# Performance work log

Measured on AMD Instinct MI355X. Metric: run time of the kernel, lower is better.

The kernel has to match this reference:

```python
import jax, jax.numpy as jnp
from jax import lax
import numpy as np

RADIUS = 0.1
NSAMPLE = 32
STRIDE = 4
NUM_DIR = 32
BN_EPS = 1e-5


def _fps(p, m):
    # furthest point sampling: p (B,N,3) -> (B,m) int32 indices, start at index 0
    B, N, _ = p.shape

    def step(carry, _):
        dists, last = carry
        lp = jnp.take_along_axis(p, jnp.broadcast_to(last[:, None, None], (B, 1, 3)), axis=1)
        d = jnp.sum((p - lp) ** 2, axis=-1)
        dists = jnp.minimum(dists, d)
        nxt = jnp.argmax(dists, axis=-1).astype(jnp.int32)
        return (dists, nxt), nxt

    last0 = jnp.zeros((B,), jnp.int32)
    d0 = jnp.full((B, N), 1e10, p.dtype)
    _, rest = lax.scan(step, (d0, last0), None, length=m - 1)
    return jnp.concatenate([last0[None, :], rest], axis=0).T  # (B, m)


def _ball_query(q, p, k, radius):
    # q (B,M,3) centers, p (B,N,3) support -> (B,M,k) indices of first k points in ball,
    # padded with the first found index (PointNet++ convention)
    N = p.shape[1]
    d2 = jnp.sum((q[:, :, None, :] - p[:, None, :, :]) ** 2, axis=-1)  # (B,M,N)
    cand = jnp.where(d2 < radius * radius, jnp.arange(N, dtype=jnp.int32), N)
    cand = jnp.sort(cand, axis=-1)[:, :, :k]
    first = cand[:, :, :1]
    return jnp.where(cand == N, first, cand)


def _bn(x, g, b, m, v):
    # BatchNorm1d eval mode on (B,C,N)
    return (x - m[:, None]) * (g[:, None] / jnp.sqrt(v[:, None] + BN_EPS)) + b[:, None]


def _normalize(x, axis):
    return x / jnp.maximum(jnp.linalg.norm(x, axis=axis, keepdims=True), 1e-12)


def setup_inputs() -> dict:
    key = jax.random.key(0)
    ks = jax.random.split(key, 16)
    B, N, Cin, Cout = 4, 8192, 128, 256
    half = Cout // 2
    s = 0.02
    return {
        "p": jax.random.uniform(ks[0], (B, N, 3), jnp.float32),
        "f": jax.random.normal(ks[1], (B, Cin, N), jnp.float32),
        "conv1_w": jax.random.normal(ks[2], (Cout, Cin), jnp.float32) * s,
        "conv1_b": jax.random.normal(ks[3], (Cout,), jnp.float32) * s,
        "skip_w": jax.random.normal(ks[4], (Cout, Cin), jnp.float32) * s,
        "skip_b": jax.random.normal(ks[5], (Cout,), jnp.float32) * s,
        "bn1_g": jnp.ones((Cout,), jnp.float32),
        "bn1_b": jnp.zeros((Cout,), jnp.float32),
        "bn1_m": jax.random.normal(ks[6], (Cout,), jnp.float32) * 0.1,
        "bn1_v": jax.random.uniform(ks[7], (Cout,), jnp.float32) + 0.5,
        "dir_vectors": jax.random.normal(ks[8], (NUM_DIR, 3), jnp.float32),
        "de_w1": jax.random.normal(ks[9], (half, NUM_DIR), jnp.float32) * s,
        "de_g": jnp.ones((half,), jnp.float32),
        "de_bb": jnp.zeros((half,), jnp.float32),
        "de_m": jax.random.normal(ks[10], (half,), jnp.float32) * 0.1,
        "de_v": jax.random.uniform(ks[11], (half,), jnp.float32) + 0.5,
        "de_w2": jax.random.normal(ks[12], (Cout, half), jnp.float32) * s,
        "de_b2": jax.random.normal(ks[13], (Cout,), jnp.float32) * s,
    }


def reference(p, f, conv1_w, conv1_b, skip_w, skip_b, bn1_g, bn1_b, bn1_m, bn1_v,
              dir_vectors, de_w1, de_g, de_bb, de_m, de_v, de_w2, de_b2):
    B, N, _ = p.shape
    Cout = conv1_w.shape[0]
    M, K = N // STRIDE, NSAMPLE

    # FPS sampling + centroid gather
    idx = _fps(p, M)  # (B,M)
    new_p = jnp.take_along_axis(p, jnp.broadcast_to(idx[:, :, None], (B, M, 3)), axis=1)

    # residual branch: gather input feats at centroids, 1x1 conv (bn_after=False)
    fi = jnp.take_along_axis(f, jnp.broadcast_to(idx[:, None, :], (B, f.shape[1], M)), axis=2)
    identity = jnp.einsum('oc,bcm->bom', skip_w, fi) + skip_b[:, None]

    # convs1: 1x1 conv on all N points
    f1 = jnp.einsum('oc,bcn->bon', conv1_w, f) + conv1_b[:, None]  # (B,Cout,N)

    # ball-query grouping
    qidx = _ball_query(new_p, p, K, RADIUS)  # (B,M,K)
    idxf = qidx.reshape(B, M * K)
    gp = jnp.take_along_axis(p, jnp.broadcast_to(idxf[:, :, None], (B, M * K, 3)), axis=1).reshape(B, M, K, 3)
    dp = jnp.transpose(gp - new_p[:, :, None, :], (0, 3, 1, 2))  # (B,3,M,K)
    fj = jnp.take_along_axis(f1, jnp.broadcast_to(idxf[:, None, :], (B, Cout, M * K)), axis=2).reshape(B, Cout, M, K)

    # directional encoding
    dpn = _normalize(dp, axis=1)
    vec = _normalize(dir_vectors, axis=1)  # (NUM_DIR,3)
    theta = jnp.einsum('md,bdnk->bmnk', vec, dpn)  # (B,NUM_DIR,M,K)
    tmax = theta.max(axis=-1)  # (B,NUM_DIR,M)
    h = jnp.einsum('om,bmn->bon', de_w1, tmax)
    h = jax.nn.gelu(_bn(h, de_g, de_bb, de_m, de_v), approximate=False)
    pe = jnp.einsum('oc,bcn->bon', de_w2, h) + de_b2[:, None]

    # neighbor max-pool + BN + residuals
    f_out = _bn(fj.max(axis=-1), bn1_g, bn1_b, bn1_m, bn1_v) + pe + identity
    return new_p, f_out
```

## Files before the change

### kernel.cpp

```cpp
#include <hip/hip_runtime.h>

#define BATCH 4
#define NPTS 8192
#define MPTS 2048
#define CIN 128
#define CO 256
#define KS 32
#define ND 32
#define HALF 128

typedef unsigned int u32;
typedef unsigned long long u64;

#define DPPC_QUAD_XOR1 0xB1
#define DPPC_QUAD_XOR2 0x4E
#define DPPC_ROW_MIRROR 0x140
#define DPPC_ROW_HALF_MIRROR 0x141
#define DPPC_ROW_BCAST15 0x142
#define DPPC_ROW_BCAST31 0x143

template<int CTRL>
__device__ __forceinline__ float dpp_max(float v) {
    int o = __builtin_amdgcn_update_dpp(__float_as_int(-1e30f), __float_as_int(v),
                                        CTRL, 0xF, 0xF, false);
    return fmaxf(v, __int_as_float(o));
}
__device__ __forceinline__ float wave_max_f32(float v) {
    v = dpp_max<DPPC_QUAD_XOR1>(v);
    v = dpp_max<DPPC_QUAD_XOR2>(v);
    v = dpp_max<DPPC_ROW_HALF_MIRROR>(v);
    v = dpp_max<DPPC_ROW_MIRROR>(v);
    v = dpp_max<DPPC_ROW_BCAST15>(v);
    v = dpp_max<DPPC_ROW_BCAST31>(v);
    return __int_as_float(__builtin_amdgcn_readlane(__float_as_int(v), 63));
}

__global__
__attribute__((amdgpu_flat_work_group_size(512, 512), amdgpu_waves_per_eu(2, 2)))
void k_fps_f1(
    const float* __restrict__ p, const float* __restrict__ f,
    const float* __restrict__ conv1_w, const float* __restrict__ conv1_b,
    float* __restrict__ out_newp, int* __restrict__ idx,
    float* __restrict__ f1t) {
    if (blockIdx.x < 4) {
        __shared__ u64 wkey[2][8];
        int b = blockIdx.x, t = threadIdx.x;
        int lane = t & 63, wid = t >> 6;
        int j0 = t * 16;
        const float* pb = p + (size_t)b * NPTS * 3;
        const float* pt = pb + t * 48;
        float px[16], py[16], pz[16], dist[16];
#pragma unroll
        for (int c = 0; c < 4; ++c) {
            float4 q0 = *(const float4*)(pt + c * 12 + 0);
            float4 q1 = *(const float4*)(pt + c * 12 + 4);
            float4 q2 = *(const float4*)(pt + c * 12 + 8);
            px[c*4+0] = q0.x; py[c*4+0] = q0.y; pz[c*4+0] = q0.z;
            px[c*4+1] = q0.w; py[c*4+1] = q1.x; pz[c*4+1] = q1.y;
            px[c*4+2] = q1.z; py[c*4+2] = q1.w; pz[c*4+2] = q2.x;
            px[c*4+3] = q2.y; py[c*4+3] = q2.z; pz[c*4+3] = q2.w;
        }
#pragma unroll
        for (int i = 0; i < 16; ++i) {
            asm volatile("" : "+v"(px[i]), "+v"(py[i]), "+v"(pz[i]));
        }
#pragma unroll
        for (int i = 0; i < 16; ++i) dist[i] = 1e10f;
        float lx = pb[0], ly = pb[1], lz = pb[2];
        if (t == 0) {
            out_newp[(size_t)b * MPTS * 3 + 0] = lx;
            out_newp[(size_t)b * MPTS * 3 + 1] = ly;
            out_newp[(size_t)b * MPTS * 3 + 2] = lz;
            idx[b * MPTS] = 0;
        }
        for (int s = 1; s < MPTS; ++s) {
            int par = s & 1;
            float bv = -1e30f; int bi = 0;
#pragma unroll
            for (int i = 0; i < 16; ++i) {
                float dx = __fsub_rn(px[i], lx);
                float dy = __fsub_rn(py[i], ly);
                float dz = __fsub_rn(pz[i], lz);
                float d  = __fadd_rn(__fadd_rn(__fmul_rn(dx, dx), __fmul_rn(dy, dy)),
                                     __fmul_rn(dz, dz));
                float nd = fminf(dist[i], d);
                dist[i] = nd;
                bool gt = nd > bv;
                bi = gt ? i : bi;
                bv = fmaxf(bv, nd);
            }
            float gmw = wave_max_f32(bv);
            u64 mask = __ballot(bv == gmw);
            int first = __ffsll((long long)mask) - 1;
            if (lane == first) {
                wkey[par][wid] = ((u64)__float_as_uint(gmw) << 32)
                               | (u64)(u32)(NPTS - 1 - (j0 + bi));
            }
            __syncthreads();
            u64 bestk = wkey[par][0];
#pragma unroll
            for (int ww = 1; ww < 8; ++ww) {
                u64 kk = wkey[par][ww];
                if (kk > bestk) bestk = kk;
            }
            int w0 = (NPTS - 1 - (int)(bestk & 0xFFFFFFFFull)) & (NPTS - 1);
            int w0s = __builtin_amdgcn_readfirstlane(w0);
            lx = pb[w0s * 3 + 0]; ly = pb[w0s * 3 + 1]; lz = pb[w0s * 3 + 2];
            if (t == 0) {
                idx[b * MPTS + s] = w0s;
                out_newp[((size_t)b * MPTS + s) * 3 + 0] = lx;
                out_newp[((size_t)b * MPTS + s) * 3 + 1] = ly;
                out_newp[((size_t)b * MPTS + s) * 3 + 2] = lz;
            }
        }
    } else if (f1t != nullptr) {
        __shared__ __align__(16) float fT[CIN * 32];
        int blk = blockIdx.x - 4;
        int b = blk >> 8;
        int n0 = (blk & 255) << 5;
        int t = threadIdx.x;
        const float* fb = f + (size_t)b * CIN * NPTS;
        for (int e = t; e < CIN * 32; e += 512) {
            int k = e >> 5, j = e & 31;
            fT[e] = fb[(size_t)k * NPTS + n0 + j];
        }
        __syncthreads();
        int c = t & 255, jh = (t >> 8) << 4;
        float bias = conv1_b[c];
        float acc[16];
#pragma unroll
        for (int j = 0; j < 16; ++j) acc[j] = bias;
        const float4* wrow4 = (const float4*)(conv1_w + (size_t)c * CIN);
        const float4* fT4 = (const float4*)fT;
        for (int k4 = 0; k4 < 32; ++k4) {
            float4 wv = wrow4[k4];
#pragma unroll
            for (int sub = 0; sub < 4; ++sub) {
                float w = sub == 0 ? wv.x : sub == 1 ? wv.y : sub == 2 ? wv.z : wv.w;
                int k = k4 * 4 + sub;
                int base = (k * 32 + jh) >> 2;
                float4 a0 = fT4[base+0], a1 = fT4[base+1], a2 = fT4[base+2], a3 = fT4[base+3];
                acc[0]  = fmaf(w, a0.x, acc[0]);  acc[1]  = fmaf(w, a0.y, acc[1]);
                acc[2]  = fmaf(w, a0.z, acc[2]);  acc[3]  = fmaf(w, a0.w, acc[3]);
                acc[4]  = fmaf(w, a1.x, acc[4]);  acc[5]  = fmaf(w, a1.y, acc[5]);
                acc[6]  = fmaf(w, a1.z, acc[6]);  acc[7]  = fmaf(w, a1.w, acc[7]);
                acc[8]  = fmaf(w, a2.x, acc[8]);  acc[9]  = fmaf(w, a2.y, acc[9]);
                acc[10] = fmaf(w, a2.z, acc[10]); acc[11] = fmaf(w, a2.w, acc[11]);
                acc[12] = fmaf(w, a3.x, acc[12]); acc[13] = fmaf(w, a3.y, acc[13]);
                acc[14] = fmaf(w, a3.z, acc[14]); acc[15] = fmaf(w, a3.w, acc[15]);
            }
        }
        float* dst = f1t + ((size_t)b * NPTS + n0 + jh) * CO + c;
#pragma unroll
        for (int j = 0; j < 16; ++j) dst[(size_t)j * CO] = acc[j];
    }
}

__global__ __launch_bounds__(256) void k_f1(const float* __restrict__ f,
                                            const float* __restrict__ conv1_w,
                                            const float* __restrict__ conv1_b,
                                            float* __restrict__ f1t, int b0) {
    __shared__ __align__(16) float fT[CIN * 16];
    int blk = blockIdx.x;
    int bl = blk >> 9;
    int b = b0 + bl;
    int n0 = (blk & 511) << 4;
    int t = threadIdx.x;
    const float* fb = f + (size_t)b * CIN * NPTS;
    for (int e = t; e < CIN * 16; e += 256) {
        int k = e >> 4, j = e & 15;
        fT[e] = fb[(size_t)k * NPTS + n0 + j];
    }
    __syncthreads();
    int c = t;
    float bias = conv1_b[c];
    float acc[16];
#pragma unroll
    for (int j = 0; j < 16; ++j) acc[j] = bias;
    const float4* wrow4 = (const float4*)(conv1_w + (size_t)c * CIN);
    const float4* fT4 = (const float4*)fT;
    for (int k4 = 0; k4 < 32; ++k4) {
        float4 wv = wrow4[k4];
#pragma unroll
        for (int sub = 0; sub < 4; ++sub) {
            float w = sub == 0 ? wv.x : sub == 1 ? wv.y : sub == 2 ? wv.z : wv.w;
            int k = k4 * 4 + sub;
            float4 a0 = fT4[k*4+0], a1 = fT4[k*4+1], a2 = fT4[k*4+2], a3 = fT4[k*4+3];
            acc[0]  = fmaf(w, a0.x, acc[0]);  acc[1]  = fmaf(w, a0.y, acc[1]);
            acc[2]  = fmaf(w, a0.z, acc[2]);  acc[3]  = fmaf(w, a0.w, acc[3]);
            acc[4]  = fmaf(w, a1.x, acc[4]);  acc[5]  = fmaf(w, a1.y, acc[5]);
            acc[6]  = fmaf(w, a1.z, acc[6]);  acc[7]  = fmaf(w, a1.w, acc[7]);
            acc[8]  = fmaf(w, a2.x, acc[8]);  acc[9]  = fmaf(w, a2.y, acc[9]);
            acc[10] = fmaf(w, a2.z, acc[10]); acc[11] = fmaf(w, a2.w, acc[11]);
            acc[12] = fmaf(w, a3.x, acc[12]); acc[13] = fmaf(w, a3.y, acc[13]);
            acc[14] = fmaf(w, a3.z, acc[14]); acc[15] = fmaf(w, a3.w, acc[15]);
        }
    }
    float* dst = f1t + ((size_t)bl * NPTS + n0) * CO + c;
#pragma unroll
    for (int j = 0; j < 16; ++j) dst[(size_t)j * CO] = acc[j];
}

__global__ __launch_bounds__(256) void k_feat(
    const float* __restrict__ p, const float* __restrict__ f,
    const float* __restrict__ f1t,
    const float* __restrict__ skip_w,  const float* __restrict__ skip_b,
    const float* __restrict__ bn1_g, const float* __restrict__ bn1_b,
    const float* __restrict__ bn1_m, const float* __restrict__ bn1_v,
    const float* __restrict__ dirv,  const float* __restrict__ de_w1,
    const float* __restrict__ de_g,  const float* __restrict__ de_bb,
    const float* __restrict__ de_m,  const float* __restrict__ de_v,
    const float* __restrict__ de_w2, const float* __restrict__ de_b2,
    const int* __restrict__ idx,     float* __restrict__ out_f, int b0) {
    __shared__ float sdx[KS], sdy[KS], sdz[KS];
    __shared__ float ltm[ND], lfi[CIN], lh[HALF];
    __shared__ int swidx[4][KS];
    __shared__ int scnt[4];
    __shared__ int nb[KS], nbp[KS];

    int q = b0 * MPTS + blockIdx.x;
    int b = q >> 11;
    int bl = b - b0;
    int m = q & (MPTS - 1);
    int t = threadIdx.x, lane = t & 63, w = t >> 6;
    const float* pb = p + (size_t)b * NPTS * 3;
    int i0 = idx[q] & (NPTS - 1);
    float qx = pb[i0 * 3 + 0], qy = pb[i0 * 3 + 1], qz = pb[i0 * 3 + 2];
    const float R2 = 0.1f * 0.1f;

    int cnt = 0;
    int seg = w * 2048;
    for (int base = 0; base < 2048; base += 64) {
        int j = seg + base + lane;
        float dx = __fsub_rn(pb[j * 3 + 0], qx);
        float dy = __fsub_rn(pb[j * 3 + 1], qy);
        float dz = __fsub_rn(pb[j * 3 + 2], qz);
        float d2 = __fadd_rn(__fadd_rn(__fmul_rn(dx, dx), __fmul_rn(dy, dy)),
                             __fmul_rn(dz, dz));
        bool hit = d2 < R2;
        u64 mask = __ballot(hit);
        if (hit) {
            int pos = cnt + __popcll(mask & ((1ull << lane) - 1ull));
            if (pos < KS) swidx[w][pos] = j;
        }
        cnt += __popcll(mask);
        if (cnt >= KS) break;
    }
    if (lane == 0) scnt[w] = cnt < KS ? cnt : KS;
    __syncthreads();
    int c0s = scnt[0], c1s = scnt[1], c2s = scnt[2], c3s = scnt[3];
    int st1 = c0s, st2 = c0s + c1s, st3 = c0s + c1s + c2s;
    int total = c0s + c1s + c2s + c3s; if (total > KS) total = KS;
    if (total < 1) total = 1;
    if (t < 128) {
        int ww = t >> 5, l = t & 31;
        int stw = (ww == 0) ? 0 : (ww == 1) ? st1 : (ww == 2) ? st2 : st3;
        int cw  = (ww == 0) ? c0s : (ww == 1) ? c1s : (ww == 2) ? c2s : c3s;
        int gp = stw + l;
        if (l < cw && gp < KS) nb[gp] = swidx[ww][l];
    }
    __syncthreads();
    if (t < KS) {
        int jk = nb[t < total ? t : 0] & (NPTS - 1);
        nbp[t] = jk;
        float dx = pb[jk * 3 + 0] - qx;
        float dy = pb[jk * 3 + 1] - qy;
        float dz = pb[jk * 3 + 2] - qz;
        float nr = fmaxf(sqrtf(dx * dx + dy * dy + dz * dz), 1e-12f);
        sdx[t] = dx / nr; sdy[t] = dy / nr; sdz[t] = dz / nr;
    }
    if (t >= 128) {
        lfi[t - 128] = f[((size_t)b * CIN + (t - 128)) * NPTS + i0];
    }
    __syncthreads();
    if (t < ND) {
        float ax = dirv[t * 3], ay = dirv[t * 3 + 1], az = dirv[t * 3 + 2];
        float n = fmaxf(sqrtf(ax * ax + ay * ay + az * az), 1e-12f);
        float vx = ax / n, vy = ay / n, vz = az / n;
        float tm = -1e30f;
#pragma unroll
        for (int k = 0; k < KS; ++k)
            tm = fmaxf(tm, vx * sdx[k] + vy * sdy[k] + vz * sdz[k]);
        ltm[t] = tm;
    }
    __syncthreads();

    int c = t;
    const float* f1b = f1t + (size_t)bl * NPTS * CO + c;
    float mx = -1e30f;
#pragma unroll 8
    for (int k = 0; k < KS; ++k) {
        mx = fmaxf(mx, f1b[(size_t)nbp[k] * CO]);
    }
    float sc1 = bn1_g[c] / sqrtf(bn1_v[c] + 1e-5f);
    float o1 = (mx - bn1_m[c]) * sc1 + bn1_b[c];

    float idv = skip_b[c];
    {
        const float4* sr = (const float4*)(skip_w + (size_t)c * CIN);
#pragma unroll 8
        for (int r = 0; r < 32; ++r) {
            float4 v = sr[r];
            idv = fmaf(v.x, lfi[r*4+0], fmaf(v.y, lfi[r*4+1],
                  fmaf(v.z, lfi[r*4+2], fmaf(v.w, lfi[r*4+3], idv))));
        }
    }
    {
        int hc = c & (HALF - 1);
        const float4* d1 = (const float4*)(de_w1 + (size_t)hc * ND);
        float a = 0.0f;
#pragma unroll
        for (int r = 0; r < 8; ++r) {
            float4 v = d1[r];
            a = fmaf(v.x, ltm[r*4+0], fmaf(v.y, ltm[r*4+1],
                fmaf(v.z, ltm[r*4+2], fmaf(v.w, ltm[r*4+3], a))));
        }
        float dsc = de_g[hc] / sqrtf(de_v[hc] + 1e-5f);
        float xb = (a - de_m[hc]) * dsc + de_bb[hc];
        float hv = 0.5f * xb * (1.0f + erff(xb * 0.70710678118654752440f));
        if (c < HALF) lh[c] = hv;
    }
    __syncthreads();
    float pe = de_b2[c];
    {
        const float4* d2p = (const float4*)(de_w2 + (size_t)c * HALF);
#pragma unroll 8
        for (int r = 0; r < 32; ++r) {
            float4 v = d2p[r];
            pe = fmaf(v.x, lh[r*4+0], fmaf(v.y, lh[r*4+1],
                 fmaf(v.z, lh[r*4+2], fmaf(v.w, lh[r*4+3], pe))));
        }
    }
    out_f[((size_t)b * CO + c) * MPTS + m] = o1 + pe + idv;
}

__global__ __launch_bounds__(256) void k_featz_fused(
    const float* __restrict__ p, const float* __restrict__ f,
    const float* __restrict__ conv1_w, const float* __restrict__ conv1_b,
    const float* __restrict__ skip_w,  const float* __restrict__ skip_b,
    const float* __restrict__ bn1_g, const float* __restrict__ bn1_b,
    const float* __restrict__ bn1_m, const float* __restrict__ bn1_v,
    const float* __restrict__ dirv,  const float* __restrict__ de_w1,
    const float* __restrict__ de_g,  const float* __restrict__ de_bb,
    const float* __restrict__ de_m,  const float* __restrict__ de_v,
    const float* __restrict__ de_w2, const float* __restrict__ de_b2,
    const int* __restrict__ idx,     float* __restrict__ out_f) {
    __shared__ __align__(16) float fg[KS * CIN];
    __shared__ float sdx[KS], sdy[KS], sdz[KS];
    __shared__ float ltm[ND], lfi[CIN], lh[HALF];
    __shared__ int swidx[4][KS];
    __shared__ int scnt[4];
    __shared__ int nb[KS], nbp[KS];

    int q = blockIdx.x;
    int b = q >> 11;
    int m = q & (MPTS - 1);
    int t = threadIdx.x, lane = t & 63, w = t >> 6;
    const float* pb = p + (size_t)b * NPTS * 3;
    int i0 = idx[q] & (NPTS - 1);
    float qx = pb[i0 * 3 + 0], qy = pb[i0 * 3 + 1], qz = pb[i0 * 3 + 2];
    const float R2 = 0.1f * 0.1f;
    int cnt = 0;
    int seg = w * 2048;
    for (int base = 0; base < 2048; base += 64) {
        int j = seg + base + lane;
        float dx = __fsub_rn(pb[j * 3 + 0], qx);
        float dy = __fsub_rn(pb[j * 3 + 1], qy);
        float dz = __fsub_rn(pb[j * 3 + 2], qz);
        float d2 = __fadd_rn(__fadd_rn(__fmul_rn(dx, dx), __fmul_rn(dy, dy)),
                             __fmul_rn(dz, dz));
        bool hit = d2 < R2;
        u64 mask = __ballot(hit);
        if (hit) {
            int pos = cnt + __popcll(mask & ((1ull << lane) - 1ull));
            if (pos < KS) swidx[w][pos] = j;
        }
        cnt += __popcll(mask);
        if (cnt >= KS) break;
    }
    if (lane == 0) scnt[w] = cnt < KS ? cnt : KS;
    __syncthreads();
    int c0s = scnt[0], c1s = scnt[1], c2s = scnt[2], c3s = scnt[3];
    int st1 = c0s, st2 = c0s + c1s, st3 = c0s + c1s + c2s;
    int total = c0s + c1s + c2s + c3s; if (total > KS) total = KS;
    if (total < 1) total = 1;
    if (t < 128) {
        int ww = t >> 5, l = t & 31;
        int stw = (ww == 0) ? 0 : (ww == 1) ? st1 : (ww == 2) ? st2 : st3;
        int cw  = (ww == 0) ? c0s : (ww == 1) ? c1s : (ww == 2) ? c2s : c3s;
        int gp = stw + l;
        if (l < cw && gp < KS) nb[gp] = swidx[ww][l];
    }
    __syncthreads();
    if (t < KS) {
        int jk = nb[t < total ? t : 0] & (NPTS - 1);
        nbp[t] = jk;
        float dx = pb[jk * 3 + 0] - qx;
        float dy = pb[jk * 3 + 1] - qy;
        float dz = pb[jk * 3 + 2] - qz;
        float nr = fmaxf(sqrtf(dx * dx + dy * dy + dz * dz), 1e-12f);
        sdx[t] = dx / nr; sdy[t] = dy / nr; sdz[t] = dz / nr;
    }
    if (t >= 128) lfi[t - 128] = f[((size_t)b * CIN + (t - 128)) * NPTS + i0];
    __syncthreads();
    if (t < ND) {
        float ax = dirv[t * 3], ay = dirv[t * 3 + 1], az = dirv[t * 3 + 2];
        float n = fmaxf(sqrtf(ax * ax + ay * ay + az * az), 1e-12f);
        float vx = ax / n, vy = ay / n, vz = az / n;
        float tm = -1e30f;
#pragma unroll
        for (int k = 0; k < KS; ++k)
            tm = fmaxf(tm, vx * sdx[k] + vy * sdy[k] + vz * sdz[k]);
        ltm[t] = tm;
    }
    for (int e = t; e < KS * CIN; e += 256) {
        int k = e >> 7, i = e & 127;
        fg[k * CIN + i] = f[((size_t)b * CIN + i) * NPTS + nbp[k]];
    }
    __syncthreads();
    int c = t;
    float acc[KS];
#pragma unroll
    for (int k = 0; k < KS; ++k) acc[k] = 0.0f;
    const float4* w4 = (const float4*)(conv1_w + (size_t)c * CIN);
    const float4* fg4 = (const float4*)fg;
    for (int i4 = 0; i4 < 32; ++i4) {
        float4 wv = w4[i4];
#pragma unroll 8
        for (int k = 0; k < KS; ++k) {
            float4 g = fg4[k * 32 + i4];
            acc[k] = fmaf(wv.x, g.x, fmaf(wv.y, g.y,
                     fmaf(wv.z, g.z, fmaf(wv.w, g.w, acc[k]))));
        }
    }
    float bias = conv1_b[c];
    float mx = -1e30f;
#pragma unroll
    for (int k = 0; k < KS; ++k) mx = fmaxf(mx, acc[k] + bias);
    float sc1 = bn1_g[c] / sqrtf(bn1_v[c] + 1e-5f);
    float o1 = (mx - bn1_m[c]) * sc1 + bn1_b[c];
    float idv = skip_b[c];
    {
        const float4* sr = (const float4*)(skip_w + (size_t)c * CIN);
#pragma unroll 8
        for (int r = 0; r < 32; ++r) {
            float4 v = sr[r];
            idv = fmaf(v.x, lfi[r*4+0], fmaf(v.y, lfi[r*4+1],
                  fmaf(v.z, lfi[r*4+2], fmaf(v.w, lfi[r*4+3], idv))));
        }
    }
    {
        int hc = c & (HALF - 1);
        const float4* d1 = (const float4*)(de_w1 + (size_t)hc * ND);
        float a = 0.0f;
#pragma unroll
        for (int r = 0; r < 8; ++r) {
            float4 v = d1[r];
            a = fmaf(v.x, ltm[r*4+0], fmaf(v.y, ltm[r*4+1],
                fmaf(v.z, ltm[r*4+2], fmaf(v.w, ltm[r*4+3], a))));
        }
        float dsc = de_g[hc] / sqrtf(de_v[hc] + 1e-5f);
        float xb = (a - de_m[hc]) * dsc + de_bb[hc];
        float hv = 0.5f * xb * (1.0f + erff(xb * 0.70710678118654752440f));
        if (c < HALF) lh[c] = hv;
    }
    __syncthreads();
    float pe = de_b2[c];
    {
        const float4* d2p = (const float4*)(de_w2 + (size_t)c * HALF);
#pragma unroll 8
        for (int r = 0; r < 32; ++r) {
            float4 v = d2p[r];
            pe = fmaf(v.x, lh[r*4+0], fmaf(v.y, lh[r*4+1],
                 fmaf(v.z, lh[r*4+2], fmaf(v.w, lh[r*4+3], pe))));
        }
    }
    out_f[((size_t)b * CO + c) * MPTS + m] = o1 + pe + idv;
}

extern "C" void kernel_launch(void* const* d_in, const int* in_sizes, int n_in,
                              void* d_out, int out_size, void* d_ws, size_t ws_size,
                              hipStream_t stream) {
    const float* p       = (const float*)d_in[0];
    const float* f       = (const float*)d_in[1];
    const float* conv1_w = (const float*)d_in[2];
    const float* conv1_b = (const float*)d_in[3];
    const float* skip_w  = (const float*)d_in[4];
    const float* skip_b  = (const float*)d_in[5];
    const float* bn1_g   = (const float*)d_in[6];
    const float* bn1_b   = (const float*)d_in[7];
    const float* bn1_m   = (const float*)d_in[8];
    const float* bn1_v   = (const float*)d_in[9];
    const float* dirv    = (const float*)d_in[10];
    const float* de_w1   = (const float*)d_in[11];
    const float* de_g    = (const float*)d_in[12];
    const float* de_bb   = (const float*)d_in[13];
    const float* de_m    = (const float*)d_in[14];
    const float* de_v    = (const float*)d_in[15];
    const float* de_w2   = (const float*)d_in[16];
    const float* de_b2   = (const float*)d_in[17];

    float* out_newp = (float*)d_out;
    float* out_f    = (float*)d_out + (size_t)BATCH * MPTS * 3;
    int*   idx      = (int*)d_ws;
    float* f1t      = (float*)((char*)d_ws + 32768);

    size_t f1_one  = (size_t)NPTS * CO * 4;
    size_t need_full = 32768 + 4 * f1_one;
    size_t need_one  = 32768 + f1_one;
    int mode = (ws_size >= need_full) ? 2 : (ws_size >= need_one) ? 1 : 0;

    if (mode == 2) {
        k_fps_f1<<<dim3(4 + 1024), dim3(512), 0, stream>>>(
            p, f, conv1_w, conv1_b, out_newp, idx, f1t);
        k_feat<<<dim3(4 * MPTS), dim3(256), 0, stream>>>(
            p, f, f1t, skip_w, skip_b, bn1_g, bn1_b, bn1_m, bn1_v,
            dirv, de_w1, de_g, de_bb, de_m, de_v, de_w2, de_b2, idx, out_f, 0);
    } else if (mode == 1) {
        k_fps_f1<<<dim3(4), dim3(512), 0, stream>>>(
            p, f, conv1_w, conv1_b, out_newp, idx, nullptr);
        for (int b0 = 0; b0 < BATCH; ++b0) {
            k_f1  <<<dim3(512),  dim3(256), 0, stream>>>(f, conv1_w, conv1_b, f1t, b0);
            k_feat<<<dim3(MPTS), dim3(256), 0, stream>>>(
                p, f, f1t, skip_w, skip_b, bn1_g, bn1_b, bn1_m, bn1_v,
                dirv, de_w1, de_g, de_bb, de_m, de_v, de_w2, de_b2, idx, out_f, b0);
        }
    } else {
        k_fps_f1<<<dim3(4), dim3(512), 0, stream>>>(
            p, f, conv1_w, conv1_b, out_newp, idx, nullptr);
        k_featz_fused<<<dim3(BATCH * MPTS), dim3(256), 0, stream>>>(
            p, f, conv1_w, conv1_b, skip_w, skip_b, bn1_g, bn1_b, bn1_m, bn1_v,
            dirv, de_w1, de_g, de_bb, de_m, de_v, de_w2, de_b2, idx, out_f);
    }
}
```

Baseline: 2.843 ms.

## Process two batches per FPS block to share barriers and interleave latency

Furthest point sampling now runs two batch items in one 512-thread block instead of one item per block, with separate shared-memory key slots for each. Each step does both reductions and shares a single __syncthreads, so the two independent dependency chains can overlap their latencies. The cost is doubled register pressure (coordinates and distances for two batches per thread) and half as many FPS blocks, which could serialize work if the two per-batch chains cannot actually hide each other's latency.

```diff
diff --git a/kernel.cpp b/kernel.cpp
--- a/kernel.cpp
+++ b/kernel.cpp
@@ -42,80 +42,134 @@
     const float* __restrict__ conv1_w, const float* __restrict__ conv1_b,
     float* __restrict__ out_newp, int* __restrict__ idx,
     float* __restrict__ f1t) {
-    if (blockIdx.x < 4) {
-        __shared__ u64 wkey[2][8];
-        int b = blockIdx.x, t = threadIdx.x;
+    if (blockIdx.x < 2) {
+        __shared__ u64 wkeyA[2][8], wkeyB[2][8];
+        int bA = (int)blockIdx.x * 2, bB = bA + 1;
+        int t = threadIdx.x;
         int lane = t & 63, wid = t >> 6;
         int j0 = t * 16;
-        const float* pb = p + (size_t)b * NPTS * 3;
-        const float* pt = pb + t * 48;
-        float px[16], py[16], pz[16], dist[16];
+        const float* pbA = p + (size_t)bA * NPTS * 3;
+        const float* pbB = p + (size_t)bB * NPTS * 3;
+        const float* ptA = pbA + t * 48;
+        const float* ptB = pbB + t * 48;
+        float pxA[16], pyA[16], pzA[16], dA[16];
+        float pxB[16], pyB[16], pzB[16], dB[16];
 #pragma unroll
         for (int c = 0; c < 4; ++c) {
-            float4 q0 = *(const float4*)(pt + c * 12 + 0);
-            float4 q1 = *(const float4*)(pt + c * 12 + 4);
-            float4 q2 = *(const float4*)(pt + c * 12 + 8);
-            px[c*4+0] = q0.x; py[c*4+0] = q0.y; pz[c*4+0] = q0.z;
-            px[c*4+1] = q0.w; py[c*4+1] = q1.x; pz[c*4+1] = q1.y;
-            px[c*4+2] = q1.z; py[c*4+2] = q1.w; pz[c*4+2] = q2.x;
-            px[c*4+3] = q2.y; py[c*4+3] = q2.z; pz[c*4+3] = q2.w;
+            float4 q0 = *(const float4*)(ptA + c * 12 + 0);
+            float4 q1 = *(const float4*)(ptA + c * 12 + 4);
+            float4 q2 = *(const float4*)(ptA + c * 12 + 8);
+            pxA[c*4+0] = q0.x; pyA[c*4+0] = q0.y; pzA[c*4+0] = q0.z;
+            pxA[c*4+1] = q0.w; pyA[c*4+1] = q1.x; pzA[c*4+1] = q1.y;
+            pxA[c*4+2] = q1.z; pyA[c*4+2] = q1.w; pzA[c*4+2] = q2.x;
+            pxA[c*4+3] = q2.y; pyA[c*4+3] = q2.z; pzA[c*4+3] = q2.w;
+        }
+#pragma unroll
+        for (int c = 0; c < 4; ++c) {
+            float4 q0 = *(const float4*)(ptB + c * 12 + 0);
+            float4 q1 = *(const float4*)(ptB + c * 12 + 4);
+            float4 q2 = *(const float4*)(ptB + c * 12 + 8);
+            pxB[c*4+0] = q0.x; pyB[c*4+0] = q0.y; pzB[c*4+0] = q0.z;
+            pxB[c*4+1] = q0.w; pyB[c*4+1] = q1.x; pzB[c*4+1] = q1.y;
+            pxB[c*4+2] = q1.z; pyB[c*4+2] = q1.w; pzB[c*4+2] = q2.x;
+            pxB[c*4+3] = q2.y; pyB[c*4+3] = q2.z; pzB[c*4+3] = q2.w;
         }
 #pragma unroll
         for (int i = 0; i < 16; ++i) {
-            asm volatile("" : "+v"(px[i]), "+v"(py[i]), "+v"(pz[i]));
-        }
-#pragma unroll
-        for (int i = 0; i < 16; ++i) dist[i] = 1e10f;
-        float lx = pb[0], ly = pb[1], lz = pb[2];
+            asm volatile("" : "+v"(pxA[i]), "+v"(pyA[i]), "+v"(pzA[i]));
+            asm volatile("" : "+v"(pxB[i]), "+v"(pyB[i]), "+v"(pzB[i]));
+        }
+#pragma unroll
+        for (int i = 0; i < 16; ++i) { dA[i] = 1e10f; dB[i] = 1e10f; }
+        float lxA = pbA[0], lyA = pbA[1], lzA = pbA[2];
+        float lxB = pbB[0], lyB = pbB[1], lzB = pbB[2];
         if (t == 0) {
-            out_newp[(size_t)b * MPTS * 3 + 0] = lx;
-            out_newp[(size_t)b * MPTS * 3 + 1] = ly;
-            out_newp[(size_t)b * MPTS * 3 + 2] = lz;
-            idx[b * MPTS] = 0;
+            out_newp[(size_t)bA * MPTS * 3 + 0] = lxA;
+            out_newp[(size_t)bA * MPTS * 3 + 1] = lyA;
+            out_newp[(size_t)bA * MPTS * 3 + 2] = lzA;
+            idx[bA * MPTS] = 0;
+            out_newp[(size_t)bB * MPTS * 3 + 0] = lxB;
+            out_newp[(size_t)bB * MPTS * 3 + 1] = lyB;
+            out_newp[(size_t)bB * MPTS * 3 + 2] = lzB;
+            idx[bB * MPTS] = 0;
         }
         for (int s = 1; s < MPTS; ++s) {
             int par = s & 1;
-            float bv = -1e30f; int bi = 0;
+            float bvA = -1e30f; int biA = 0;
 #pragma unroll
             for (int i = 0; i < 16; ++i) {
-                float dx = __fsub_rn(px[i], lx);
-                float dy = __fsub_rn(py[i], ly);
-                float dz = __fsub_rn(pz[i], lz);
+                float dx = __fsub_rn(pxA[i], lxA);
+                float dy = __fsub_rn(pyA[i], lyA);
+                float dz = __fsub_rn(pzA[i], lzA);
                 float d  = __fadd_rn(__fadd_rn(__fmul_rn(dx, dx), __fmul_rn(dy, dy)),
                                      __fmul_rn(dz, dz));
-                float nd = fminf(dist[i], d);
-                dist[i] = nd;
-                bool gt = nd > bv;
-                bi = gt ? i : bi;
-                bv = fmaxf(bv, nd);
-            }
-            float gmw = wave_max_f32(bv);
-            u64 mask = __ballot(bv == gmw);
-            int first = __ffsll((long long)mask) - 1;
-            if (lane == first) {
-                wkey[par][wid] = ((u64)__float_as_uint(gmw) << 32)
-                               | (u64)(u32)(NPTS - 1 - (j0 + bi));
+                float nd = fminf(dA[i], d);
+                dA[i] = nd;
+                bool gt = nd > bvA;
+                biA = gt ? i : biA;
+                bvA = fmaxf(bvA, nd);
+            }
+            float gmwA = wave_max_f32(bvA);
+            u64 maskA = __ballot(bvA == gmwA);
+            int firstA = __ffsll((long long)maskA) - 1;
+            if (lane == firstA) {
+                wkeyA[par][wid] = ((u64)__float_as_uint(gmwA) << 32)
+                                | (u64)(u32)(NPTS - 1 - (j0 + biA));
+            }
+            float bvB = -1e30f; int biB = 0;
+#pragma unroll
+            for (int i = 0; i < 16; ++i) {
+                float dx = __fsub_rn(pxB[i], lxB);
+                float dy = __fsub_rn(pyB[i], lyB);
+                float dz = __fsub_rn(pzB[i], lzB);
+                float d  = __fadd_rn(__fadd_rn(__fmul_rn(dx, dx), __fmul_rn(dy, dy)),
+                                     __fmul_rn(dz, dz));
+                float nd = fminf(dB[i], d);
+                dB[i] = nd;
+                bool gt = nd > bvB;
+                biB = gt ? i : biB;
+                bvB = fmaxf(bvB, nd);
+            }
+            float gmwB = wave_max_f32(bvB);
+            u64 maskB = __ballot(bvB == gmwB);
+            int firstB = __ffsll((long long)maskB) - 1;
+            if (lane == firstB) {
+                wkeyB[par][wid] = ((u64)__float_as_uint(gmwB) << 32)
+                                | (u64)(u32)(NPTS - 1 - (j0 + biB));
             }
             __syncthreads();
-            u64 bestk = wkey[par][0];
+            u64 bestkA = wkeyA[par][0];
 #pragma unroll
             for (int ww = 1; ww < 8; ++ww) {
-                u64 kk = wkey[par][ww];
-                if (kk > bestk) bestk = kk;
-            }
-            int w0 = (NPTS - 1 - (int)(bestk & 0xFFFFFFFFull)) & (NPTS - 1);
-            int w0s = __builtin_amdgcn_readfirstlane(w0);
-            lx = pb[w0s * 3 + 0]; ly = pb[w0s * 3 + 1]; lz = pb[w0s * 3 + 2];
+                u64 kk = wkeyA[par][ww];
+                if (kk > bestkA) bestkA = kk;
+            }
+            int w0A = (NPTS - 1 - (int)(bestkA & 0xFFFFFFFFull)) & (NPTS - 1);
+            int w0As = __builtin_amdgcn_readfirstlane(w0A);
+            lxA = pbA[w0As * 3 + 0]; lyA = pbA[w0As * 3 + 1]; lzA = pbA[w0As * 3 + 2];
+            u64 bestkB = wkeyB[par][0];
+#pragma unroll
+            for (int ww = 1; ww < 8; ++ww) {
+                u64 kk = wkeyB[par][ww];
+                if (kk > bestkB) bestkB = kk;
+            }
+            int w0B = (NPTS - 1 - (int)(bestkB & 0xFFFFFFFFull)) & (NPTS - 1);
+            int w0Bs = __builtin_amdgcn_readfirstlane(w0B);
+            lxB = pbB[w0Bs * 3 + 0]; lyB = pbB[w0Bs * 3 + 1]; lzB = pbB[w0Bs * 3 + 2];
             if (t == 0) {
-                idx[b * MPTS + s] = w0s;
-                out_newp[((size_t)b * MPTS + s) * 3 + 0] = lx;
-                out_newp[((size_t)b * MPTS + s) * 3 + 1] = ly;
-                out_newp[((size_t)b * MPTS + s) * 3 + 2] = lz;
+                idx[bA * MPTS + s] = w0As;
+                out_newp[((size_t)bA * MPTS + s) * 3 + 0] = lxA;
+                out_newp[((size_t)bA * MPTS + s) * 3 + 1] = lyA;
+                out_newp[((size_t)bA * MPTS + s) * 3 + 2] = lzA;
+                idx[bB * MPTS + s] = w0Bs;
+                out_newp[((size_t)bB * MPTS + s) * 3 + 0] = lxB;
+                out_newp[((size_t)bB * MPTS + s) * 3 + 1] = lyB;
+                out_newp[((size_t)bB * MPTS + s) * 3 + 2] = lzB;
             }
         }
     } else if (f1t != nullptr) {
         __shared__ __align__(16) float fT[CIN * 32];
-        int blk = blockIdx.x - 4;
+        int blk = blockIdx.x - 2;
         int b = blk >> 8;
         int n0 = (blk & 255) << 5;
         int t = threadIdx.x;
@@ -511,13 +565,13 @@
     int mode = (ws_size >= need_full) ? 2 : (ws_size >= need_one) ? 1 : 0;
 
     if (mode == 2) {
-        k_fps_f1<<<dim3(4 + 1024), dim3(512), 0, stream>>>(
+        k_fps_f1<<<dim3(2 + 1024), dim3(512), 0, stream>>>(
             p, f, conv1_w, conv1_b, out_newp, idx, f1t);
         k_feat<<<dim3(4 * MPTS), dim3(256), 0, stream>>>(
             p, f, f1t, skip_w, skip_b, bn1_g, bn1_b, bn1_m, bn1_v,
             dirv, de_w1, de_g, de_bb, de_m, de_v, de_w2, de_b2, idx, out_f, 0);
     } else if (mode == 1) {
-        k_fps_f1<<<dim3(4), dim3(512), 0, stream>>>(
+        k_fps_f1<<<dim3(2), dim3(512), 0, stream>>>(
             p, f, conv1_w, conv1_b, out_newp, idx, nullptr);
         for (int b0 = 0; b0 < BATCH; ++b0) {
             k_f1  <<<dim3(512),  dim3(256), 0, stream>>>(f, conv1_w, conv1_b, f1t, b0);
@@ -526,7 +580,7 @@
                 dirv, de_w1, de_g, de_bb, de_m, de_v, de_w2, de_b2, idx, out_f, b0);
         }
     } else {
-        k_fps_f1<<<dim3(4), dim3(512), 0, stream>>>(
+        k_fps_f1<<<dim3(2), dim3(512), 0, stream>>>(
             p, f, conv1_w, conv1_b, out_newp, idx, nullptr);
         k_featz_fused<<<dim3(BATCH * MPTS), dim3(256), 0, stream>>>(
             p, f, conv1_w, conv1_b, skip_w, skip_b, bn1_g, bn1_b, bn1_m, bn1_v,
```

Result: slower. 5.078 ms (+78.6%).
